# Kernel tuning notes

Hardware: AMD Instinct MI355X
Metric: run time of the kernel (lower is better)

The kernel has to match this reference:

```python
import jax, jax.numpy as jnp
import numpy as np

WINDOW = (1, 7, 7)
DIM_HEAD = 32


def _rel_pos_index(ws):
    d, h, w = ws
    coords = np.stack(np.meshgrid(np.arange(d), np.arange(h), np.arange(w), indexing='ij'))
    cf = coords.reshape(3, -1)                      # [3, N]
    rel = (cf[:, :, None] - cf[:, None, :]).transpose(1, 2, 0).copy()  # [N, N, 3]
    rel[..., 0] += d - 1
    rel[..., 1] += h - 1
    rel[..., 2] += w - 1
    rel[..., 0] *= (2 * h - 1) * (2 * w - 1)
    rel[..., 1] *= (2 * w - 1)
    return jnp.asarray(rel.sum(-1))                 # [N, N] int32, N = 49


REL_IDX = _rel_pos_index(WINDOW)


def setup_inputs() -> dict:
    key = jax.random.key(0)
    k1, k2, k3, k4, k5 = jax.random.split(key, 5)
    B, X, Y, W1, W2, D = 4, 32, 32, 7, 7, 512
    heads = D // DIM_HEAD
    n_bias = (2 * WINDOW[0] - 1) * (2 * WINDOW[1] - 1) * (2 * WINDOW[2] - 1)  # 169
    s = 1.0 / np.sqrt(D)
    return {
        'x': jax.random.normal(k1, (B, X, Y, W1, W2, D), jnp.float32),
        'y': jax.random.normal(k2, (B, X, Y, W1, W2, D), jnp.float32),
        'Wq': jax.random.normal(k3, (D, D), jnp.float32) * s,
        'Wkv': jax.random.normal(k4, (D, 2 * D), jnp.float32) * s,
        'bias_table': jax.random.normal(k5, (n_bias, heads), jnp.float32) * 0.02,
    }


def reference(x, y, Wq, Wkv, bias_table):
    B, X, Y, W1, W2, D = x.shape
    h = D // DIM_HEAD
    n = W1 * W2                                     # 49 tokens per window
    scale = DIM_HEAD ** -0.5

    xr = x.reshape(B * X * Y, n, D)                 # [Bw, n, D]
    yr = y.reshape(B * X * Y, n, D)

    q = xr @ Wq                                     # [Bw, n, D]
    kv = yr @ Wkv                                   # [Bw, n, 2D]
    k, v = kv[..., :D], kv[..., D:]

    def to_heads(t):
        return t.reshape(t.shape[0], n, h, DIM_HEAD).transpose(0, 2, 1, 3)  # [Bw, h, n, dh]

    q, k, v = to_heads(q), to_heads(k), to_heads(v)

    sim = jnp.einsum('bhid,bhjd->bhij', q, k) * scale   # [Bw, h, n, n]
    bias = bias_table[REL_IDX]                          # [n, n, h]
    sim = sim + bias.transpose(2, 0, 1)[None]           # broadcast over windows

    attn = jax.nn.softmax(sim, axis=-1)
    out = jnp.einsum('bhij,bhjd->bhid', attn, v)        # [Bw, h, n, dh]
    out = out.transpose(0, 2, 1, 3).reshape(B * X * Y, W1, W2, D)
    return out.reshape(B, X, Y, W1, W2, D)
```

## Files before the change

kernel.cpp:

```cpp
#include <hip/hip_runtime.h>


typedef __bf16 bf16x8 __attribute__((ext_vector_type(8)));
typedef __attribute__((ext_vector_type(4))) float f32x4;

#define DEVI __device__ __forceinline__

DEVI unsigned short f2bf(float f) {
  union { float f; unsigned u; } v; v.f = f;
  unsigned r = v.u + 0x7FFFu + ((v.u >> 16) & 1u);
  return (unsigned short)(r >> 16);
}
DEVI unsigned pkbf(float a, float b) {
  return (unsigned)f2bf(a) | ((unsigned)f2bf(b) << 16);
}

#define MFMA16(a, b, c) __builtin_amdgcn_mfma_f32_16x16x32_bf16((a), (b), (c), 0, 0, 0)

#define SWZ_Y(r)  ((((unsigned)(r)) & 7u) << 4)
#define SWZ_A(r)  (((((unsigned)(r)) >> 2) & 3u) << 5)
#define SWZ_P(r)  ((((unsigned)(r)) & 7u) << 4)
#define SWZ_VT(r) ((((unsigned)(r)) & 7u) << 4)

__global__ void prep_kernel(const float* __restrict__ Wq, const float* __restrict__ Wkv,
                            const float* __restrict__ bt, char* __restrict__ ws) {
  int t = blockIdx.x * 256 + threadIdx.x;
  if (t < 786432) {
    int e = t & 7, lane = (t >> 3) & 63, ks = (t >> 9) & 15, nt = (t >> 13) & 1,
        h = (t >> 14) & 15, T = t >> 18;
    int row = ks * 32 + (lane >> 4) * 8 + e;
    int col = h * 32 + nt * 16 + (lane & 15);
    float v;
    if (T == 0)      v = Wq[row * 512 + col] * 0.17677669529663687f;
    else if (T == 1) v = Wkv[row * 1024 + col];
    else             v = Wkv[row * 1024 + 512 + col];
    ((unsigned short*)ws)[t] = f2bf(v);
  }
  if (t < 262144) {
    int r = t & 3, lane = (t >> 2) & 63, jt = (t >> 8) & 3, it = (t >> 10) & 3,
        h = (t >> 12) & 15;
    int i = it * 16 + (lane & 15);
    int j = jt * 16 + ((lane >> 4) & 3) * 4 + r;
    float v;
    if (j >= 49)      v = -1e30f;
    else if (i >= 49) v = 0.0f;
    else {
      int hi = i / 7, wi = i % 7, hj = j / 7, wj = j % 7;
      v = bt[((hi - hj + 6) * 13 + (wi - wj + 6)) * 16 + h];
    }
    ((float*)(ws + 1572864))[t] = v;
  }
}

DEVI bf16x8 ldXY(const char* base, int row, int kc) {
  unsigned a = ((unsigned)(row * 1024 + kc * 2)) ^ SWZ_Y(row);
  return *(const bf16x8*)(base + a);
}
DEVI bf16x8 ldXY_c(const char* base, int row, int kc) {
  int rc = row < 48 ? row : 48;
  bf16x8 v = ldXY(base, rc, kc);
  if (row > 48) {
    union { long long z[2]; bf16x8 v; } u; u.z[0] = 0; u.z[1] = 0;
    v = u.v;
  }
  return v;
}
DEVI bf16x8 ldQK(const char* base, int row, int kc) {
  int rc = row < 48 ? row : 48;
  unsigned a = ((unsigned)(rc * 64 + kc * 2)) ^ SWZ_A(rc);
  return *(const bf16x8*)(base + a);
}
DEVI bf16x8 ldP2(const char* base, int row, int jc) {
  int rc = row < 48 ? row : 48;
  unsigned a = ((unsigned)(rc * 128 + jc * 2)) ^ SWZ_P(rc);
  return *(const bf16x8*)(base + a);
}
DEVI bf16x8 ldVT(const char* base, int dh, int jc) {
  unsigned a = ((unsigned)(dh * 128 + jc * 2)) ^ SWZ_VT(dh);
  return *(const bf16x8*)(base + a);
}

__global__ __launch_bounds__(512, 2)
void attn_kernel(const float* __restrict__ x, const float* __restrict__ y,
                 const char* __restrict__ wsW, const float* __restrict__ biasD,
                 float* __restrict__ out) {
  extern __shared__ char smem[];
  char* xb = smem;
  char* yb = smem + 50176;
  const int tid = threadIdx.x;
  const int lane = tid & 63, wave = tid >> 6;
  const int p = wave >> 1, sub = wave & 1;
  const int g = lane >> 4, lr = lane & 15;
  char* pbase = smem + 100352 + p * 10368;
  char* qb = pbase;
  char* kb = pbase + 3136;
  char* vt = pbase + 6272;
  char* Pb = pbase;

  const int bw = blockIdx.x;
  const float* xs = x + (size_t)bw * 25088;
  const float* ys = y + (size_t)bw * 25088;

  for (int it = tid; it < 6272; it += 512) {
    float4 v = ((const float4*)xs)[it];
    float4 w = ((const float4*)ys)[it];
    int i = it >> 7;
    int k = (it & 127) << 2;
    unsigned a = ((unsigned)(i * 1024 + k * 2)) ^ SWZ_Y(i);
    uint2 ux, uy;
    ux.x = pkbf(v.x, v.y); ux.y = pkbf(v.z, v.w);
    uy.x = pkbf(w.x, w.y); uy.y = pkbf(w.z, w.w);
    *(uint2*)(xb + a) = ux;
    *(uint2*)(yb + a) = uy;
  }

  const bf16x8* wsQ = (const bf16x8*)wsW;
  const bf16x8* wsK = (const bf16x8*)(wsW + 524288);
  const bf16x8* wsV = (const bf16x8*)(wsW + 1048576);
  const f32x4* bD = (const f32x4*)biasD;
  const f32x4 fz = {0.f, 0.f, 0.f, 0.f};

  for (int hi = 0; hi < 4; ++hi) {
    const int h = p * 4 + hi;

    __syncthreads();

    f32x4 accq[4];
    #pragma unroll
    for (int mt = 0; mt < 4; ++mt) accq[mt] = fz;
    {
      const bf16x8* pQ = wsQ + (size_t)((h * 2 + sub) * 16) * 64 + lane;
      bf16x8 bq[16];
      #pragma unroll
      for (int ks = 0; ks < 16; ++ks) bq[ks] = pQ[ks * 64];
      #pragma unroll
      for (int ks = 0; ks < 16; ++ks) {
        int kc = ks * 32 + g * 8;
        accq[0] = MFMA16(ldXY(xb, lr, kc),        bq[ks], accq[0]);
        accq[1] = MFMA16(ldXY(xb, lr + 16, kc),   bq[ks], accq[1]);
        accq[2] = MFMA16(ldXY(xb, lr + 32, kc),   bq[ks], accq[2]);
        accq[3] = MFMA16(ldXY_c(xb, lr + 48, kc), bq[ks], accq[3]);
      }
    }
    #pragma unroll
    for (int mt = 0; mt < 4; ++mt)
      #pragma unroll
      for (int r = 0; r < 4; ++r) {
        int row = mt * 16 + g * 4 + r;
        if (row < 49) {
          unsigned a = ((unsigned)(row * 64 + (sub * 16 + lr) * 2)) ^ SWZ_A(row);
          *(unsigned short*)(qb + a) = f2bf(accq[mt][r]);
        }
      }

    f32x4 acck[4], accv[4];
    #pragma unroll
    for (int mt = 0; mt < 4; ++mt) { acck[mt] = fz; accv[mt] = fz; }
    {
      const bf16x8* pK = wsK + (size_t)((h * 2 + sub) * 16) * 64 + lane;
      const bf16x8* pV = wsV + (size_t)((h * 2 + sub) * 16) * 64 + lane;
      bf16x8 ksr[8], vsr[8];
      #pragma unroll
      for (int i = 0; i < 8; ++i) { ksr[i] = pK[i * 64]; vsr[i] = pV[i * 64]; }
      #pragma unroll
      for (int ks = 0; ks < 16; ++ks) {
        bf16x8 bk = ksr[ks & 7], bv = vsr[ks & 7];
        if (ks < 8) {
          ksr[ks & 7] = pK[(ks + 8) * 64];
          vsr[ks & 7] = pV[(ks + 8) * 64];
        }
        int kc = ks * 32 + g * 8;
        bf16x8 a0 = ldXY(yb, lr, kc);
        bf16x8 a1 = ldXY(yb, lr + 16, kc);
        bf16x8 a2 = ldXY(yb, lr + 32, kc);
        bf16x8 a3 = ldXY_c(yb, lr + 48, kc);
        acck[0] = MFMA16(a0, bk, acck[0]);
        acck[1] = MFMA16(a1, bk, acck[1]);
        acck[2] = MFMA16(a2, bk, acck[2]);
        acck[3] = MFMA16(a3, bk, acck[3]);
        accv[0] = MFMA16(a0, bv, accv[0]);
        accv[1] = MFMA16(a1, bv, accv[1]);
        accv[2] = MFMA16(a2, bv, accv[2]);
        accv[3] = MFMA16(a3, bv, accv[3]);
      }
    }
    #pragma unroll
    for (int mt = 0; mt < 4; ++mt) {
      #pragma unroll
      for (int r = 0; r < 4; ++r) {
        int row = mt * 16 + g * 4 + r;
        if (row < 49) {
          unsigned a = ((unsigned)(row * 64 + (sub * 16 + lr) * 2)) ^ SWZ_A(row);
          *(unsigned short*)(kb + a) = f2bf(acck[mt][r]);
        }
      }
      int dh = sub * 16 + lr;
      int t0 = mt * 16 + g * 4;
      unsigned a = ((unsigned)(dh * 128 + t0 * 2)) ^ SWZ_VT(dh);
      uint2 pk;
      pk.x = pkbf(accv[mt][0], accv[mt][1]);
      pk.y = pkbf(accv[mt][2], accv[mt][3]);
      *(uint2*)(vt + a) = pk;
    }

    __syncthreads();

    f32x4 bias[2][4];
    #pragma unroll
    for (int mi = 0; mi < 2; ++mi)
      #pragma unroll
      for (int jt = 0; jt < 4; ++jt)
        bias[mi][jt] = bD[(size_t)(((h * 4 + sub * 2 + mi) * 4 + jt) * 64 + lane)];

    bf16x8 qa[2], kf[4];
    #pragma unroll
    for (int mi = 0; mi < 2; ++mi) qa[mi] = ldQK(qb, sub * 32 + mi * 16 + lr, g * 8);
    #pragma unroll
    for (int jt = 0; jt < 4; ++jt) kf[jt] = ldQK(kb, jt * 16 + lr, g * 8);
    f32x4 accs[2][4];
    #pragma unroll
    for (int mi = 0; mi < 2; ++mi)
      #pragma unroll
      for (int jt = 0; jt < 4; ++jt)
        accs[mi][jt] = MFMA16(kf[jt], qa[mi], fz);

    uint2 pks[2][4];
    #pragma unroll
    for (int mi = 0; mi < 2; ++mi) {
      f32x4 vals[4];
      #pragma unroll
      for (int jt = 0; jt < 4; ++jt) vals[jt] = accs[mi][jt] + bias[mi][jt];
      float m = vals[0][0];
      #pragma unroll
      for (int jt = 0; jt < 4; ++jt)
        #pragma unroll
        for (int r = 0; r < 4; ++r) m = fmaxf(m, vals[jt][r]);
      m = fmaxf(m, __shfl_xor(m, 16));
      m = fmaxf(m, __shfl_xor(m, 32));
      float s = 0.f;
      #pragma unroll
      for (int jt = 0; jt < 4; ++jt)
        #pragma unroll
        for (int r = 0; r < 4; ++r) {
          float pv = __expf(vals[jt][r] - m);
          vals[jt][r] = pv;
          s += pv;
        }
      s += __shfl_xor(s, 16);
      s += __shfl_xor(s, 32);
      float inv = 1.0f / s;
      #pragma unroll
      for (int jt = 0; jt < 4; ++jt) {
        pks[mi][jt].x = pkbf(vals[jt][0] * inv, vals[jt][1] * inv);
        pks[mi][jt].y = pkbf(vals[jt][2] * inv, vals[jt][3] * inv);
      }
    }

    __syncthreads();

    #pragma unroll
    for (int mi = 0; mi < 2; ++mi) {
      int i = sub * 32 + mi * 16 + lr;
      if (i < 49) {
        #pragma unroll
        for (int jt = 0; jt < 4; ++jt) {
          unsigned a = ((unsigned)(i * 128 + (jt * 16 + g * 4) * 2)) ^ SWZ_P(i);
          *(uint2*)(Pb + a) = pks[mi][jt];
        }
      }
    }

    f32x4 acco[2][2];
    acco[0][0] = fz; acco[0][1] = fz; acco[1][0] = fz; acco[1][1] = fz;
    #pragma unroll
    for (int ks = 0; ks < 2; ++ks) {
      int jc = ks * 32 + g * 8;
      bf16x8 av0 = ldVT(vt, lr, jc);
      bf16x8 av1 = ldVT(vt, lr + 16, jc);
      bf16x8 bp0 = ldP2(Pb, sub * 32 + lr, jc);
      bf16x8 bp1 = ldP2(Pb, sub * 32 + 16 + lr, jc);
      acco[0][0] = MFMA16(av0, bp0, acco[0][0]);
      acco[0][1] = MFMA16(av0, bp1, acco[0][1]);
      acco[1][0] = MFMA16(av1, bp0, acco[1][0]);
      acco[1][1] = MFMA16(av1, bp1, acco[1][1]);
    }

    float* ow = out + (size_t)bw * 25088 + h * 32;
    #pragma unroll
    for (int it = 0; it < 2; ++it) {
      int tok = sub * 32 + it * 16 + lr;
      if (tok < 49) {
        #pragma unroll
        for (int md = 0; md < 2; ++md)
          *(f32x4*)(&ow[(size_t)tok * 512 + md * 16 + g * 4]) = acco[md][it];
      }
    }
  }
}

extern "C" void kernel_launch(void* const* d_in, const int* in_sizes, int n_in,
                              void* d_out, int out_size, void* d_ws, size_t ws_size,
                              hipStream_t stream) {
  (void)in_sizes; (void)n_in; (void)out_size; (void)ws_size;
  const float* x = (const float*)d_in[0];
  const float* y = (const float*)d_in[1];
  const float* Wq = (const float*)d_in[2];
  const float* Wkv = (const float*)d_in[3];
  const float* bt = (const float*)d_in[4];
  float* out = (float*)d_out;
  char* ws = (char*)d_ws;

  prep_kernel<<<3072, 256, 0, stream>>>(Wq, Wkv, bt, ws);

  (void)hipFuncSetAttribute((const void*)attn_kernel,
                            hipFuncAttributeMaxDynamicSharedMemorySize, 141824);
  attn_kernel<<<4096, 512, 141824, stream>>>(x, y, (const char*)ws,
                                             (const float*)(ws + 1572864), out);
}
```

Before: 709.5 us.

## Double waves per block and split projection tiles 2x2 across waves

The attention kernel now launches with 1024 threads, i.e. 16 waves per block instead of 8. Each group of four waves shares one head's LDS region. Within a group the Q/K/V projection is split into 2x2 tiles over token rows and head-dim halves, and each wave handles one 16-row query tile in the score, softmax and PV steps. The aim is more resident waves per CU to hide LDS and global latency, and a lighter per-wave register load. In exchange, weight fragments are fetched twice per group, and the tighter launch bounds may cap registers and cause spills.

```diff
diff --git a/kernel.cpp b/kernel.cpp
--- a/kernel.cpp
+++ b/kernel.cpp
@@ -80,7 +80,7 @@
   return *(const bf16x8*)(base + a);
 }
 
-__global__ __launch_bounds__(512, 2)
+__global__ __launch_bounds__(1024, 4)
 void attn_kernel(const float* __restrict__ x, const float* __restrict__ y,
                  const char* __restrict__ wsW, const float* __restrict__ biasD,
                  float* __restrict__ out) {
@@ -89,9 +89,9 @@
   char* yb = smem + 50176;
   const int tid = threadIdx.x;
   const int lane = tid & 63, wave = tid >> 6;
-  const int p = wave >> 1, sub = wave & 1;
+  const int quad = wave >> 2, m2 = (wave >> 1) & 1, n2 = wave & 1, iw = wave & 3;
   const int g = lane >> 4, lr = lane & 15;
-  char* pbase = smem + 100352 + p * 10368;
+  char* pbase = smem + 100352 + quad * 10368;
   char* qb = pbase;
   char* kb = pbase + 3136;
   char* vt = pbase + 6272;
@@ -101,7 +101,7 @@
   const float* xs = x + (size_t)bw * 25088;
   const float* ys = y + (size_t)bw * 25088;
 
-  for (int it = tid; it < 6272; it += 512) {
+  for (int it = tid; it < 6272; it += 1024) {
     float4 v = ((const float4*)xs)[it];
     float4 w = ((const float4*)ys)[it];
     int i = it >> 7;
@@ -120,45 +120,48 @@
   const f32x4* bD = (const f32x4*)biasD;
   const f32x4 fz = {0.f, 0.f, 0.f, 0.f};
 
+  const int r0 = m2 * 32 + lr;
+  const int r1 = m2 * 32 + 16 + lr;
+
   for (int hi = 0; hi < 4; ++hi) {
-    const int h = p * 4 + hi;
+    const int h = quad * 4 + hi;
 
     __syncthreads();
 
-    f32x4 accq[4];
-    #pragma unroll
-    for (int mt = 0; mt < 4; ++mt) accq[mt] = fz;
-    {
-      const bf16x8* pQ = wsQ + (size_t)((h * 2 + sub) * 16) * 64 + lane;
-      bf16x8 bq[16];
-      #pragma unroll
-      for (int ks = 0; ks < 16; ++ks) bq[ks] = pQ[ks * 64];
+    f32x4 accq[2];
+    accq[0] = fz; accq[1] = fz;
+    {
+      const bf16x8* pQ = wsQ + (size_t)((h * 2 + n2) * 16) * 64 + lane;
+      bf16x8 qsr[8];
+      #pragma unroll
+      for (int i = 0; i < 8; ++i) qsr[i] = pQ[i * 64];
       #pragma unroll
       for (int ks = 0; ks < 16; ++ks) {
+        bf16x8 bq = qsr[ks & 7];
+        if (ks < 8) qsr[ks & 7] = pQ[(ks + 8) * 64];
         int kc = ks * 32 + g * 8;
-        accq[0] = MFMA16(ldXY(xb, lr, kc),        bq[ks], accq[0]);
-        accq[1] = MFMA16(ldXY(xb, lr + 16, kc),   bq[ks], accq[1]);
-        accq[2] = MFMA16(ldXY(xb, lr + 32, kc),   bq[ks], accq[2]);
-        accq[3] = MFMA16(ldXY_c(xb, lr + 48, kc), bq[ks], accq[3]);
-      }
-    }
-    #pragma unroll
-    for (int mt = 0; mt < 4; ++mt)
+        bf16x8 a0 = ldXY(xb, r0, kc);
+        bf16x8 a1 = ldXY_c(xb, r1, kc);
+        accq[0] = MFMA16(a0, bq, accq[0]);
+        accq[1] = MFMA16(a1, bq, accq[1]);
+      }
+    }
+    #pragma unroll
+    for (int mt = 0; mt < 2; ++mt)
       #pragma unroll
       for (int r = 0; r < 4; ++r) {
-        int row = mt * 16 + g * 4 + r;
+        int row = m2 * 32 + mt * 16 + g * 4 + r;
         if (row < 49) {
-          unsigned a = ((unsigned)(row * 64 + (sub * 16 + lr) * 2)) ^ SWZ_A(row);
+          unsigned a = ((unsigned)(row * 64 + (n2 * 16 + lr) * 2)) ^ SWZ_A(row);
           *(unsigned short*)(qb + a) = f2bf(accq[mt][r]);
         }
       }
 
-    f32x4 acck[4], accv[4];
-    #pragma unroll
-    for (int mt = 0; mt < 4; ++mt) { acck[mt] = fz; accv[mt] = fz; }
-    {
-      const bf16x8* pK = wsK + (size_t)((h * 2 + sub) * 16) * 64 + lane;
-      const bf16x8* pV = wsV + (size_t)((h * 2 + sub) * 16) * 64 + lane;
+    f32x4 acck[2], accv[2];
+    acck[0] = fz; acck[1] = fz; accv[0] = fz; accv[1] = fz;
+    {
+      const bf16x8* pK = wsK + (size_t)((h * 2 + n2) * 16) * 64 + lane;
+      const bf16x8* pV = wsV + (size_t)((h * 2 + n2) * 16) * 64 + lane;
       bf16x8 ksr[8], vsr[8];
       #pragma unroll
       for (int i = 0; i < 8; ++i) { ksr[i] = pK[i * 64]; vsr[i] = pV[i * 64]; }
@@ -170,32 +173,26 @@
           vsr[ks & 7] = pV[(ks + 8) * 64];
         }
         int kc = ks * 32 + g * 8;
-        bf16x8 a0 = ldXY(yb, lr, kc);
-        bf16x8 a1 = ldXY(yb, lr + 16, kc);
-        bf16x8 a2 = ldXY(yb, lr + 32, kc);
-        bf16x8 a3 = ldXY_c(yb, lr + 48, kc);
+        bf16x8 a0 = ldXY(yb, r0, kc);
+        bf16x8 a1 = ldXY_c(yb, r1, kc);
         acck[0] = MFMA16(a0, bk, acck[0]);
         acck[1] = MFMA16(a1, bk, acck[1]);
-        acck[2] = MFMA16(a2, bk, acck[2]);
-        acck[3] = MFMA16(a3, bk, acck[3]);
         accv[0] = MFMA16(a0, bv, accv[0]);
         accv[1] = MFMA16(a1, bv, accv[1]);
-        accv[2] = MFMA16(a2, bv, accv[2]);
-        accv[3] = MFMA16(a3, bv, accv[3]);
-      }
-    }
-    #pragma unroll
-    for (int mt = 0; mt < 4; ++mt) {
+      }
+    }
+    #pragma unroll
+    for (int mt = 0; mt < 2; ++mt) {
       #pragma unroll
       for (int r = 0; r < 4; ++r) {
-        int row = mt * 16 + g * 4 + r;
+        int row = m2 * 32 + mt * 16 + g * 4 + r;
         if (row < 49) {
-          unsigned a = ((unsigned)(row * 64 + (sub * 16 + lr) * 2)) ^ SWZ_A(row);
+          unsigned a = ((unsigned)(row * 64 + (n2 * 16 + lr) * 2)) ^ SWZ_A(row);
           *(unsigned short*)(kb + a) = f2bf(acck[mt][r]);
         }
       }
-      int dh = sub * 16 + lr;
-      int t0 = mt * 16 + g * 4;
+      int dh = n2 * 16 + lr;
+      int t0 = m2 * 32 + mt * 16 + g * 4;
       unsigned a = ((unsigned)(dh * 128 + t0 * 2)) ^ SWZ_VT(dh);
       uint2 pk;
       pk.x = pkbf(accv[mt][0], accv[mt][1]);
@@ -205,31 +202,24 @@
 
     __syncthreads();
 
-    f32x4 bias[2][4];
-    #pragma unroll
-    for (int mi = 0; mi < 2; ++mi)
-      #pragma unroll
-      for (int jt = 0; jt < 4; ++jt)
-        bias[mi][jt] = bD[(size_t)(((h * 4 + sub * 2 + mi) * 4 + jt) * 64 + lane)];
-
-    bf16x8 qa[2], kf[4];
-    #pragma unroll
-    for (int mi = 0; mi < 2; ++mi) qa[mi] = ldQK(qb, sub * 32 + mi * 16 + lr, g * 8);
+    f32x4 bias[4];
+    #pragma unroll
+    for (int jt = 0; jt < 4; ++jt)
+      bias[jt] = bD[(size_t)(((h * 4 + iw) * 4 + jt) * 64 + lane)];
+
+    bf16x8 qa = ldQK(qb, iw * 16 + lr, g * 8);
+    bf16x8 kf[4];
     #pragma unroll
     for (int jt = 0; jt < 4; ++jt) kf[jt] = ldQK(kb, jt * 16 + lr, g * 8);
-    f32x4 accs[2][4];
-    #pragma unroll
-    for (int mi = 0; mi < 2; ++mi)
-      #pragma unroll
-      for (int jt = 0; jt < 4; ++jt)
-        accs[mi][jt] = MFMA16(kf[jt], qa[mi], fz);
-
-    uint2 pks[2][4];
-    #pragma unroll
-    for (int mi = 0; mi < 2; ++mi) {
-      f32x4 vals[4];
-      #pragma unroll
-      for (int jt = 0; jt < 4; ++jt) vals[jt] = accs[mi][jt] + bias[mi][jt];
+
+    f32x4 vals[4];
+    #pragma unroll
+    for (int jt = 0; jt < 4; ++jt) vals[jt] = MFMA16(kf[jt], qa, fz);
+    #pragma unroll
+    for (int jt = 0; jt < 4; ++jt) vals[jt] = vals[jt] + bias[jt];
+
+    uint2 pks[4];
+    {
       float m = vals[0][0];
       #pragma unroll
       for (int jt = 0; jt < 4; ++jt)
@@ -251,48 +241,43 @@
       float inv = 1.0f / s;
       #pragma unroll
       for (int jt = 0; jt < 4; ++jt) {
-        pks[mi][jt].x = pkbf(vals[jt][0] * inv, vals[jt][1] * inv);
-        pks[mi][jt].y = pkbf(vals[jt][2] * inv, vals[jt][3] * inv);
+        pks[jt].x = pkbf(vals[jt][0] * inv, vals[jt][1] * inv);
+        pks[jt].y = pkbf(vals[jt][2] * inv, vals[jt][3] * inv);
       }
     }
 
     __syncthreads();
 
-    #pragma unroll
-    for (int mi = 0; mi < 2; ++mi) {
-      int i = sub * 32 + mi * 16 + lr;
+    {
+      int i = iw * 16 + lr;
       if (i < 49) {
         #pragma unroll
         for (int jt = 0; jt < 4; ++jt) {
           unsigned a = ((unsigned)(i * 128 + (jt * 16 + g * 4) * 2)) ^ SWZ_P(i);
-          *(uint2*)(Pb + a) = pks[mi][jt];
-        }
-      }
-    }
-
-    f32x4 acco[2][2];
-    acco[0][0] = fz; acco[0][1] = fz; acco[1][0] = fz; acco[1][1] = fz;
+          *(uint2*)(Pb + a) = pks[jt];
+        }
+      }
+    }
+
+    f32x4 acco[2];
+    acco[0] = fz; acco[1] = fz;
     #pragma unroll
     for (int ks = 0; ks < 2; ++ks) {
       int jc = ks * 32 + g * 8;
       bf16x8 av0 = ldVT(vt, lr, jc);
       bf16x8 av1 = ldVT(vt, lr + 16, jc);
-      bf16x8 bp0 = ldP2(Pb, sub * 32 + lr, jc);
-      bf16x8 bp1 = ldP2(Pb, sub * 32 + 16 + lr, jc);
-      acco[0][0] = MFMA16(av0, bp0, acco[0][0]);
-      acco[0][1] = MFMA16(av0, bp1, acco[0][1]);
-      acco[1][0] = MFMA16(av1, bp0, acco[1][0]);
-      acco[1][1] = MFMA16(av1, bp1, acco[1][1]);
+      bf16x8 bp = ldP2(Pb, iw * 16 + lr, jc);
+      acco[0] = MFMA16(av0, bp, acco[0]);
+      acco[1] = MFMA16(av1, bp, acco[1]);
     }
 
     float* ow = out + (size_t)bw * 25088 + h * 32;
-    #pragma unroll
-    for (int it = 0; it < 2; ++it) {
-      int tok = sub * 32 + it * 16 + lr;
+    {
+      int tok = iw * 16 + lr;
       if (tok < 49) {
         #pragma unroll
         for (int md = 0; md < 2; ++md)
-          *(f32x4*)(&ow[(size_t)tok * 512 + md * 16 + g * 4]) = acco[md][it];
+          *(f32x4*)(&ow[(size_t)tok * 512 + md * 16 + g * 4]) = acco[md];
       }
     }
   }
@@ -314,6 +299,6 @@
 
   (void)hipFuncSetAttribute((const void*)attn_kernel,
                             hipFuncAttributeMaxDynamicSharedMemorySize, 141824);
-  attn_kernel<<<4096, 512, 141824, stream>>>(x, y, (const char*)ws,
-                                             (const float*)(ws + 1572864), out);
-}
+  attn_kernel<<<4096, 1024, 141824, stream>>>(x, y, (const char*)ws,
+                                              (const float*)(ws + 1572864), out);
+}
```

Result: slower. 851.3 us (+20.0%).
